# Kernel optimization log

Hardware: AMD Instinct MI355X
Metric: run time of the kernel (lower is better)

The kernel has to match this reference:

```python
import jax, jax.numpy as jnp
import numpy as np

NV, NE, D, NNZ = 100000, 50000, 128, 1600000
EPS = 1e-5

def _seg_mean(vals, idx, n):
    # vals: [nnz, d] gathered rows; mean-aggregate into n segments
    s = jax.ops.segment_sum(vals, idx, num_segments=n)
    c = jax.ops.segment_sum(jnp.ones((idx.shape[0], 1), vals.dtype), idx, num_segments=n)
    return s / jnp.maximum(c, 1.0)

def _linear(x, W, b):
    return x @ W.T + b

def _layer_norm(x, g, b):
    m = jnp.mean(x, axis=-1, keepdims=True)
    v = jnp.mean((x - m) ** 2, axis=-1, keepdims=True)
    return (x - m) * jax.lax.rsqrt(v + EPS) * g + b

def setup_inputs() -> dict:
    key = jax.random.key(0)
    ks = jax.random.split(key, 12)
    inp = {
        "X": jax.random.normal(ks[0], (NV, D), jnp.float32),
        "Y": jax.random.normal(ks[1], (NE, D), jnp.float32),
        "v_idx": jax.random.randint(ks[2], (NNZ,), 0, NV, jnp.int32),
        "e_idx": jax.random.randint(ks[3], (NNZ,), 0, NE, jnp.int32),
        "W_tv": jax.random.normal(ks[4], (D, D), jnp.float32) * 0.05,
        "b_tv": jnp.zeros((D,), jnp.float32),
        "W_te": jax.random.normal(ks[5], (D, D), jnp.float32) * 0.05,
        "b_te": jnp.zeros((D,), jnp.float32),
        "W_em": jax.random.normal(ks[6], (D, 2 * D), jnp.float32) * 0.05,
        "b_em": jnp.zeros((D,), jnp.float32),
        "W_vm": jax.random.normal(ks[7], (D, 2 * D), jnp.float32) * 0.05,
        "b_vm": jnp.zeros((D,), jnp.float32),
        "g_v": jnp.ones((D,), jnp.float32),
        "be_v": jnp.zeros((D,), jnp.float32),
        "g_e": jnp.ones((D,), jnp.float32),
        "be_e": jnp.zeros((D,), jnp.float32),
    }
    return inp

def reference(X, Y, v_idx, e_idx, W_tv, b_tv, W_te, b_te, W_em, b_em, W_vm, b_vm, g_v, be_v, g_e, be_e):
    X0, Y0 = X, Y
    Xp = _linear(X0, W_tv, b_tv)                       # [NV, D] theta_vertex
    # v2e aggregation (mean): gather vertex rows per incidence, reduce to edges
    msg_e = _seg_mean(Xp[v_idx], e_idx, NE)            # [NE, D]
    Ym = _linear(jnp.concatenate([Y0, msg_e], axis=-1), W_em, b_em)  # edge_merge
    Ym = _linear(Ym, W_te, b_te)                       # theta_edge
    # e2v aggregation (mean)
    msg_v = _seg_mean(Ym[e_idx], v_idx, NV)            # [NV, D]
    Xm = _linear(jnp.concatenate([X0, msg_v], axis=-1), W_vm, b_vm)  # vertex_merge
    Xo = jax.nn.relu(_layer_norm(Xm, g_v, be_v))       # dropout is identity at eval / p=0
    Yo = jax.nn.relu(_layer_norm(Ym, g_e, be_e))
    return (Xo, Yo)
```

## Files before the change

kernel.cpp:

```cpp
#include <hip/hip_runtime.h>
#include <stdint.h>

#define NVERT 100000
#define NEDGE 50000
#define DIM 128
#define NNZ_N 1600000
#define N4 (NNZ_N / 4)
#define CAP_E 96
#define CAP_V 56
#define NB_QTR 1563
#define NB_G23 782
#define MSG_STRIDE 256

typedef __attribute__((ext_vector_type(8))) short bf16x8;
typedef __attribute__((ext_vector_type(4))) float f32x4;

__device__ __forceinline__ unsigned short f32_to_bf16(float f) {
  union { float f; unsigned u; } v; v.f = f;
  unsigned r = v.u + 0x7fffu + ((v.u >> 16) & 1u);
  return (unsigned short)(r >> 16);
}
__device__ __forceinline__ float bf16_lo(unsigned u) {
  union { unsigned u; float f; } v; v.u = u << 16; return v.f;
}
__device__ __forceinline__ float bf16_hi(unsigned u) {
  union { unsigned u; float f; } v; v.u = u & 0xffff0000u; return v.f;
}
__device__ __forceinline__ float ldf(const void* p, long i, int bf) {
  if (bf) {
    union { unsigned u; float f; } v;
    v.u = (unsigned)((const unsigned short*)p)[i] << 16;
    return v.f;
  }
  return ((const float*)p)[i];
}
__device__ __forceinline__ bf16x8 frag_ext(const void* A, long idx, int bf) {
  if (bf) return *(const bf16x8*)((const unsigned short*)A + idx);
  const float* f = (const float*)A + idx;
  float4 f0 = *(const float4*)f, f1 = *(const float4*)(f + 4);
  bf16x8 r;
  r[0] = (short)f32_to_bf16(f0.x); r[1] = (short)f32_to_bf16(f0.y);
  r[2] = (short)f32_to_bf16(f0.z); r[3] = (short)f32_to_bf16(f0.w);
  r[4] = (short)f32_to_bf16(f1.x); r[5] = (short)f32_to_bf16(f1.y);
  r[6] = (short)f32_to_bf16(f1.z); r[7] = (short)f32_to_bf16(f1.w);
  return r;
}

__device__ __forceinline__ int block_flag(const unsigned short* x) {
  __shared__ int cnt;
  if (threadIdx.x == 0) cnt = 0;
  __syncthreads();
  int c = 0;
#pragma unroll
  for (int k = 0; k < 4; ++k) {
    unsigned short h = x[(threadIdx.x * 4 + k) * 2];
    int ex = (h >> 7) & 0xFF;
    c += (ex >= 100 && ex <= 140) ? 1 : 0;
  }
  atomicAdd(&cnt, c);
  __syncthreads();
  return cnt > 512;
}

__global__ __launch_bounds__(256) void prep0(
    const unsigned short* __restrict__ Xu,
    const void* __restrict__ btv, const void* __restrict__ bvm,
    const void* __restrict__ Wtv,
    float* __restrict__ btvf, float* __restrict__ bvmf,
    unsigned short* __restrict__ Wtvb, int* __restrict__ flag,
    int* __restrict__ cnt_e, int* __restrict__ cnt_v) {
  int b = blockIdx.x, t = threadIdx.x;
  if (b >= 65) {
    int i = (b - 65) * 256 + t;
    if (i < NEDGE) cnt_e[i] = 0;
    else if (i < NEDGE + NVERT) cnt_v[i - NEDGE] = 0;
    return;
  }
  int bf = block_flag(Xu);
  if (b == 0) {
    if (t == 0) flag[0] = bf;
    if (t < 128) btvf[t] = ldf(btv, t, bf);
    else bvmf[t - 128] = ldf(bvm, t - 128, bf);
  } else {
    int i = (b - 1) * 256 + t;
    Wtvb[i] = f32_to_bf16(ldf(Wtv, i, bf));
  }
}

__device__ __forceinline__ void prep_wc_body(
    int b, const void* __restrict__ Wvm, const void* __restrict__ Wte,
    const void* __restrict__ Wem, const void* __restrict__ bte,
    const void* __restrict__ bem, unsigned short* __restrict__ Wvmb,
    unsigned short* __restrict__ Wcb, float* __restrict__ bcf, int bf) {
  int t = threadIdx.x;
  if (b < 128) {
    int i = b * 256 + t;
    Wvmb[i] = f32_to_bf16(ldf(Wvm, i, bf));
  } else {
    int n = b - 128, k = t;
    float acc = 0.f;
    for (int j = 0; j < 128; ++j)
      acc += ldf(Wte, n * 128 + j, bf) * ldf(Wem, j * 256 + k, bf);
    Wcb[n * 256 + k] = f32_to_bf16(acc);
    if (k == 0) {
      float bb = ldf(bte, n, bf);
      for (int j = 0; j < 128; ++j) bb += ldf(Wte, n * 128 + j, bf) * ldf(bem, j, bf);
      bcf[n] = bb;
    }
  }
}

__device__ __forceinline__ void ecount_body(
    const int4* __restrict__ vi, const int4* __restrict__ ei,
    int* __restrict__ cnt_e, int* __restrict__ adj_e, int bid) {
  int i = bid * 256 + threadIdx.x;
  if (i >= N4) return;
  int4 e = ei[i], v = vi[i];
  int t;
  t = atomicAdd(&cnt_e[e.x], 1); if (t < CAP_E) adj_e[e.x * CAP_E + t] = v.x;
  t = atomicAdd(&cnt_e[e.y], 1); if (t < CAP_E) adj_e[e.y * CAP_E + t] = v.y;
  t = atomicAdd(&cnt_e[e.z], 1); if (t < CAP_E) adj_e[e.z * CAP_E + t] = v.z;
  t = atomicAdd(&cnt_e[e.w], 1); if (t < CAP_E) adj_e[e.w * CAP_E + t] = v.w;
}

__device__ __forceinline__ void vcount_body(
    const int4* __restrict__ vi, const int4* __restrict__ ei,
    int* __restrict__ cnt_v, unsigned short* __restrict__ adj_v, int bid) {
  int i = bid * 256 + threadIdx.x;
  if (i >= N4) return;
  int4 v = vi[i], e = ei[i];
  int t;
  t = atomicAdd(&cnt_v[v.x], 1); if (t < CAP_V) adj_v[v.x * CAP_V + t] = (unsigned short)e.x;
  t = atomicAdd(&cnt_v[v.y], 1); if (t < CAP_V) adj_v[v.y * CAP_V + t] = (unsigned short)e.y;
  t = atomicAdd(&cnt_v[v.z], 1); if (t < CAP_V) adj_v[v.z * CAP_V + t] = (unsigned short)e.z;
  t = atomicAdd(&cnt_v[v.w], 1); if (t < CAP_V) adj_v[v.w * CAP_V + t] = (unsigned short)e.w;
}

template<typename IT, int CAP>
__device__ __forceinline__ void seg_body(
    const int* __restrict__ cntp, const IT* __restrict__ adj,
    const unsigned short* __restrict__ tbl, unsigned short* __restrict__ out,
    int nseg, int nrows, int bid) {
  const int seg = (bid * 256 + threadIdx.x) >> 4;
  const int l = threadIdx.x & 15;
  if (seg >= nseg) return;
  int cnt = cntp[seg];
  int s = seg * CAP;
  int e = s + (cnt < CAP ? cnt : CAP);
  float a0 = 0, a1 = 0, a2 = 0, a3 = 0, a4 = 0, a5 = 0, a6 = 0, a7 = 0;
#define ROW(r, u)                                      \
  if ((unsigned)r >= (unsigned)nrows) r = 0;           \
  uint4 u = *(const uint4*)(tbl + (long)r * DIM + l * 8);
#define ACC(u)                                         \
  a0 += bf16_lo(u.x); a1 += bf16_hi(u.x);              \
  a2 += bf16_lo(u.y); a3 += bf16_hi(u.y);              \
  a4 += bf16_lo(u.z); a5 += bf16_hi(u.z);              \
  a6 += bf16_lo(u.w); a7 += bf16_hi(u.w);
  int i = s;
  for (; i + 8 <= e; i += 8) {
    int r0 = adj[i],     r1 = adj[i + 1], r2 = adj[i + 2], r3 = adj[i + 3];
    int r4 = adj[i + 4], r5 = adj[i + 5], r6 = adj[i + 6], r7 = adj[i + 7];
    ROW(r0, u0) ROW(r1, u1) ROW(r2, u2) ROW(r3, u3)
    ROW(r4, u4) ROW(r5, u5) ROW(r6, u6) ROW(r7, u7)
    ACC(u0) ACC(u1) ACC(u2) ACC(u3) ACC(u4) ACC(u5) ACC(u6) ACC(u7)
  }
  for (; i + 4 <= e; i += 4) {
    int r0 = adj[i], r1 = adj[i + 1], r2 = adj[i + 2], r3 = adj[i + 3];
    ROW(r0, u0) ROW(r1, u1) ROW(r2, u2) ROW(r3, u3)
    ACC(u0) ACC(u1) ACC(u2) ACC(u3)
  }
  for (; i < e; ++i) {
    int r = adj[i];
    ROW(r, u)
    ACC(u)
  }
#undef ACC
#undef ROW
  float inv = (cnt > 0) ? 1.f / (float)cnt : 0.f;
  bf16x8 r;
  r[0] = (short)f32_to_bf16(a0 * inv); r[1] = (short)f32_to_bf16(a1 * inv);
  r[2] = (short)f32_to_bf16(a2 * inv); r[3] = (short)f32_to_bf16(a3 * inv);
  r[4] = (short)f32_to_bf16(a4 * inv); r[5] = (short)f32_to_bf16(a5 * inv);
  r[6] = (short)f32_to_bf16(a6 * inv); r[7] = (short)f32_to_bf16(a7 * inv);
  *(bf16x8*)(out + (long)seg * MSG_STRIDE + l * 8) = r;
}

__device__ __forceinline__ void gemm1_body(
    int bid, const void* __restrict__ A0,
    const unsigned short* __restrict__ Bw, const float* __restrict__ biasf,
    unsigned short* __restrict__ outb, int M, int bf) {
  const int wave = threadIdx.x >> 6;
  const int lane = threadIdx.x & 63;
  const int m0 = bid * 64 + wave * 16;
  if (m0 >= M) return;
  const int c = lane & 15;
  const int q = lane >> 4;
  const long arow = m0 + c;
  f32x4 acc[8];
#pragma unroll
  for (int t = 0; t < 8; ++t) acc[t] = (f32x4){0.f, 0.f, 0.f, 0.f};
#pragma unroll
  for (int ks = 0; ks < 4; ++ks) {
    const int kk = ks * 32 + q * 8;
    bf16x8 a = frag_ext(A0, arow * 128 + kk, bf);
#pragma unroll
    for (int t = 0; t < 8; ++t) {
      bf16x8 b = *(const bf16x8*)(Bw + (long)(t * 16 + c) * 128 + kk);
      acc[t] = __builtin_amdgcn_mfma_f32_16x16x32_bf16(a, b, acc[t], 0, 0, 0);
    }
  }
#pragma unroll
  for (int t = 0; t < 8; ++t) {
    float bv = biasf[t * 16 + c];
    int col = t * 16 + c;
#pragma unroll
    for (int i = 0; i < 4; ++i)
      outb[(long)(m0 + q * 4 + i) * DIM + col] = f32_to_bf16(acc[t][i] + bv);
  }
}

template<bool STORE_BF16>
__device__ __forceinline__ void gemm23_body(
    int bid, int rowbase, int M,
    const void* __restrict__ A0, const unsigned short* __restrict__ A1b,
    const unsigned short* __restrict__ Bw, const float* __restrict__ biasf,
    unsigned short* __restrict__ outb, float* __restrict__ outf,
    const void* __restrict__ gw_, const void* __restrict__ bw_, int bf) {
  const int wave = threadIdx.x >> 6;
  const int lane = threadIdx.x & 63;
  const int m0 = rowbase + bid * 64 + wave * 16;
  if (m0 >= M) return;
  const int c = lane & 15;
  const int q = lane >> 4;
  const long arow = m0 + c;

  f32x4 acc[8];
#pragma unroll
  for (int t = 0; t < 8; ++t) acc[t] = (f32x4){0.f, 0.f, 0.f, 0.f};
#pragma unroll
  for (int ks = 0; ks < 8; ++ks) {
    const int kk = ks * 32 + q * 8;
    bf16x8 a;
    if (ks >= 4) a = *(const bf16x8*)(A1b + arow * MSG_STRIDE + (kk - 128));
    else         a = frag_ext(A0, arow * 128 + kk, bf);
#pragma unroll
    for (int t = 0; t < 8; ++t) {
      bf16x8 b = *(const bf16x8*)(Bw + (long)(t * 16 + c) * 256 + kk);
      acc[t] = __builtin_amdgcn_mfma_f32_16x16x32_bf16(a, b, acc[t], 0, 0, 0);
    }
  }
#pragma unroll
  for (int t = 0; t < 8; ++t) {
    float bv = biasf[t * 16 + c];
#pragma unroll
    for (int i = 0; i < 4; ++i) acc[t][i] += bv;
  }
  if (STORE_BF16) {
#pragma unroll
    for (int t = 0; t < 8; ++t) {
      int col = t * 16 + c;
#pragma unroll
      for (int i = 0; i < 4; ++i)
        outb[(long)(m0 + q * 4 + i) * DIM + col] = f32_to_bf16(acc[t][i]);
    }
  }
  float sum[4] = {0, 0, 0, 0}, sq[4] = {0, 0, 0, 0};
#pragma unroll
  for (int t = 0; t < 8; ++t)
#pragma unroll
    for (int i = 0; i < 4; ++i) { float v = acc[t][i]; sum[i] += v; sq[i] += v * v; }
#pragma unroll
  for (int m = 1; m <= 8; m <<= 1) {
#pragma unroll
    for (int i = 0; i < 4; ++i) {
      sum[i] += __shfl_xor(sum[i], m, 64);
      sq[i]  += __shfl_xor(sq[i], m, 64);
    }
  }
  float mean[4], rstd[4];
#pragma unroll
  for (int i = 0; i < 4; ++i) {
    mean[i] = sum[i] * (1.0f / 128.0f);
    float var = sq[i] * (1.0f / 128.0f) - mean[i] * mean[i];
    rstd[i] = rsqrtf(var + 1e-5f);
  }
#pragma unroll
  for (int t = 0; t < 8; ++t) {
    int col = t * 16 + c;
    float gv = ldf(gw_, col, bf), bv = ldf(bw_, col, bf);
#pragma unroll
    for (int i = 0; i < 4; ++i) {
      float v = (acc[t][i] - mean[i]) * rstd[i] * gv + bv;
      v = v > 0.f ? v : 0.f;
      outf[(long)(m0 + q * 4 + i) * DIM + col] = v;
    }
  }
}

__global__ __launch_bounds__(256) void k1_prep_ecount_gemm1(
    const int4* __restrict__ vi, const int4* __restrict__ ei,
    int* __restrict__ cnt_e, int* __restrict__ adj_e,
    const void* __restrict__ X, const unsigned short* __restrict__ Wtvb,
    const float* __restrict__ btvf, unsigned short* __restrict__ Xp_b,
    const void* __restrict__ Wvm, const void* __restrict__ Wte,
    const void* __restrict__ Wem, const void* __restrict__ bte,
    const void* __restrict__ bem, unsigned short* __restrict__ Wvmb,
    unsigned short* __restrict__ Wcb, float* __restrict__ bcf,
    const int* __restrict__ flagp) {
  int b = blockIdx.x;
  if (b < 256) {
    prep_wc_body(b, Wvm, Wte, Wem, bte, bem, Wvmb, Wcb, bcf, *flagp);
    return;
  }
  int b2 = b - 256;
  if (b2 & 1)
    gemm1_body(b2 >> 1, X, Wtvb, btvf, Xp_b, NVERT, *flagp);
  else
    ecount_body(vi, ei, cnt_e, adj_e, b2 >> 1);
}

__global__ __launch_bounds__(256) void k2_vcount_seg1(
    const int4* __restrict__ vi, const int4* __restrict__ ei,
    int* __restrict__ cnt_v, unsigned short* __restrict__ adj_v,
    const int* __restrict__ cnt_e, const int* __restrict__ adj_e,
    const unsigned short* __restrict__ Xp_b, unsigned short* __restrict__ msg_e) {
  int r = blockIdx.x % 3, q = blockIdx.x / 3;
  if (r == 0)
    vcount_body(vi, ei, cnt_v, adj_v, q);
  else
    seg_body<int, CAP_E>(cnt_e, adj_e, Xp_b, msg_e, NEDGE, NVERT,
                         q * 2 + (r - 1));
}

__global__ __launch_bounds__(256) void k3_gemm2(
    const void* __restrict__ Y, const unsigned short* __restrict__ msg_e,
    const unsigned short* __restrict__ Wcb, const float* __restrict__ bcf,
    unsigned short* __restrict__ Ym_b, float* __restrict__ Yo,
    const void* __restrict__ g_e, const void* __restrict__ be_e,
    const int* __restrict__ flagp) {
  gemm23_body<true>(blockIdx.x, 0, NEDGE, Y, msg_e, Wcb, bcf, Ym_b, Yo,
                    g_e, be_e, *flagp);
}

__global__ __launch_bounds__(256) void k4a_seg2(
    const int* __restrict__ cnt_v, const unsigned short* __restrict__ adj_v,
    const unsigned short* __restrict__ Ym_b, unsigned short* __restrict__ msg_v) {
  seg_body<unsigned short, CAP_V>(cnt_v, adj_v, Ym_b, msg_v, NVERT, NEDGE,
                                  blockIdx.x);
}

__global__ __launch_bounds__(256) void k4b_seg2_gemm3(
    const int* __restrict__ cnt_v, const unsigned short* __restrict__ adj_v,
    const unsigned short* __restrict__ Ym_b, unsigned short* __restrict__ msg_v,
    const void* __restrict__ X, const unsigned short* __restrict__ Wvmb,
    const float* __restrict__ bvmf, float* __restrict__ Xo,
    const void* __restrict__ g_v, const void* __restrict__ be_v,
    const int* __restrict__ flagp) {
  int r = blockIdx.x % 5, q = blockIdx.x / 5;
  if (r == 4)
    gemm23_body<false>(q, 0, NVERT / 2, X, msg_v, Wvmb, bvmf, nullptr, Xo,
                       g_v, be_v, *flagp);
  else
    seg_body<unsigned short, CAP_V>(cnt_v, adj_v, Ym_b, msg_v, NVERT, NEDGE,
                                    3125 + q * 4 + r);
}

__global__ __launch_bounds__(256) void k5_gemm3(
    const void* __restrict__ X, const unsigned short* __restrict__ msg_v,
    const unsigned short* __restrict__ Wvmb, const float* __restrict__ bvmf,
    float* __restrict__ Xo, const void* __restrict__ g_v,
    const void* __restrict__ be_v, const int* __restrict__ flagp) {
  gemm23_body<false>(blockIdx.x, NVERT / 2, NVERT, X, msg_v, Wvmb, bvmf,
                     nullptr, Xo, g_v, be_v, *flagp);
}

extern "C" void kernel_launch(void* const* d_in, const int* in_sizes, int n_in,
                              void* d_out, int out_size, void* d_ws, size_t ws_size,
                              hipStream_t stream) {
  const void* X    = d_in[0];
  const void* Y    = d_in[1];
  const int*  v_idx = (const int*)d_in[2];
  const int*  e_idx = (const int*)d_in[3];
  const void* W_tv = d_in[4];
  const void* b_tv = d_in[5];
  const void* W_te = d_in[6];
  const void* b_te = d_in[7];
  const void* W_em = d_in[8];
  const void* b_em = d_in[9];
  const void* W_vm = d_in[10];
  const void* b_vm = d_in[11];
  const void* g_v  = d_in[12];
  const void* be_v = d_in[13];
  const void* g_e  = d_in[14];
  const void* be_e = d_in[15];

  unsigned short* Xp_b  = (unsigned short*)d_out;
  int*   adj_e = (int*)((char*)d_out + 25600000);
  unsigned short* msg_e = (unsigned short*)((char*)d_out + 51200000);
  float* Yo    = (float*)((char*)d_out + 51200000);
  unsigned short* msg_v = (unsigned short*)d_out;
  float* Xo    = (float*)d_out;

  char* p = (char*)d_ws;
  auto alloc = [&](size_t n) { char* r = p; p += (n + 255) & ~(size_t)255; return r; };
  int*   flag  = (int*)alloc(4);
  float* btv_f = (float*)alloc(DIM * 4);
  float* bvm_f = (float*)alloc(DIM * 4);
  float* bc_f  = (float*)alloc(DIM * 4);
  unsigned short* Wtv_b = (unsigned short*)alloc(DIM * DIM * 2);
  unsigned short* Wvm_b = (unsigned short*)alloc(2 * DIM * DIM * 2);
  unsigned short* Wc_b  = (unsigned short*)alloc(2 * DIM * DIM * 2);
  unsigned short* Ym_b  = (unsigned short*)alloc((long)NEDGE * DIM * 2);
  int* cnt_e  = (int*)alloc(NEDGE * 4);
  int* cnt_v  = (int*)alloc(NVERT * 4);
  unsigned short* adj_v = (unsigned short*)alloc((long)NVERT * CAP_V * 2);

  prep0<<<65 + (NEDGE + NVERT + 255) / 256, 256, 0, stream>>>(
      (const unsigned short*)X, b_tv, b_vm, W_tv, btv_f, bvm_f, Wtv_b, flag,
      cnt_e, cnt_v);

  k1_prep_ecount_gemm1<<<256 + 2 * NB_QTR, 256, 0, stream>>>(
      (const int4*)v_idx, (const int4*)e_idx, cnt_e, adj_e,
      X, Wtv_b, btv_f, Xp_b,
      W_vm, W_te, W_em, b_te, b_em, Wvm_b, Wc_b, bc_f, flag);

  k2_vcount_seg1<<<3 * NB_QTR, 256, 0, stream>>>(
      (const int4*)v_idx, (const int4*)e_idx, cnt_v, adj_v,
      cnt_e, adj_e, Xp_b, msg_e);

  k3_gemm2<<<NB_G23, 256, 0, stream>>>(
      Y, msg_e, Wc_b, bc_f, Ym_b, Yo, g_e, be_e, flag);

  k4a_seg2<<<3125, 256, 0, stream>>>(cnt_v, adj_v, Ym_b, msg_v);

  k4b_seg2_gemm3<<<5 * NB_G23, 256, 0, stream>>>(
      cnt_v, adj_v, Ym_b, msg_v, X, Wvm_b, bvm_f, Xo, g_v, be_v, flag);

  k5_gemm3<<<NB_G23, 256, 0, stream>>>(
      X, msg_v, Wvm_b, bvm_f, Xo, g_v, be_v, flag);
}
```

Before: 523.1 us.

## Split vertex aggregation/merge into three staggered stages and vectorize adjacency loads

Splits the vertex-side segment aggregation and vertex-merge GEMM into three thirds. Each fused launch aggregates the next third of vertices while the GEMM processes the previous third, which shortens the serialized tail and adds one kernel launch. Adjacency indices in the gather loop are now read with 128-bit vector loads instead of scalar loads, and the 4-wide remainder loop is dropped. The atomics in the incidence-counting kernels are also issued back to back before the dependent stores, to overlap atomic latency.

```diff
diff --git a/kernel.cpp b/kernel.cpp
--- a/kernel.cpp
+++ b/kernel.cpp
@@ -11,6 +11,10 @@
 #define NB_QTR 1563
 #define NB_G23 782
 #define MSG_STRIDE 256
+#define SEG_T1 33344
+#define SEG_T2 66688
+#define SB3 2084
+#define GB3 521
 
 typedef __attribute__((ext_vector_type(8))) short bf16x8;
 typedef __attribute__((ext_vector_type(4))) float f32x4;
@@ -116,11 +120,14 @@
   int i = bid * 256 + threadIdx.x;
   if (i >= N4) return;
   int4 e = ei[i], v = vi[i];
-  int t;
-  t = atomicAdd(&cnt_e[e.x], 1); if (t < CAP_E) adj_e[e.x * CAP_E + t] = v.x;
-  t = atomicAdd(&cnt_e[e.y], 1); if (t < CAP_E) adj_e[e.y * CAP_E + t] = v.y;
-  t = atomicAdd(&cnt_e[e.z], 1); if (t < CAP_E) adj_e[e.z * CAP_E + t] = v.z;
-  t = atomicAdd(&cnt_e[e.w], 1); if (t < CAP_E) adj_e[e.w * CAP_E + t] = v.w;
+  int t0 = atomicAdd(&cnt_e[e.x], 1);
+  int t1 = atomicAdd(&cnt_e[e.y], 1);
+  int t2 = atomicAdd(&cnt_e[e.z], 1);
+  int t3 = atomicAdd(&cnt_e[e.w], 1);
+  if (t0 < CAP_E) adj_e[e.x * CAP_E + t0] = v.x;
+  if (t1 < CAP_E) adj_e[e.y * CAP_E + t1] = v.y;
+  if (t2 < CAP_E) adj_e[e.z * CAP_E + t2] = v.z;
+  if (t3 < CAP_E) adj_e[e.w * CAP_E + t3] = v.w;
 }
 
 __device__ __forceinline__ void vcount_body(
@@ -129,11 +136,14 @@
   int i = bid * 256 + threadIdx.x;
   if (i >= N4) return;
   int4 v = vi[i], e = ei[i];
-  int t;
-  t = atomicAdd(&cnt_v[v.x], 1); if (t < CAP_V) adj_v[v.x * CAP_V + t] = (unsigned short)e.x;
-  t = atomicAdd(&cnt_v[v.y], 1); if (t < CAP_V) adj_v[v.y * CAP_V + t] = (unsigned short)e.y;
-  t = atomicAdd(&cnt_v[v.z], 1); if (t < CAP_V) adj_v[v.z * CAP_V + t] = (unsigned short)e.z;
-  t = atomicAdd(&cnt_v[v.w], 1); if (t < CAP_V) adj_v[v.w * CAP_V + t] = (unsigned short)e.w;
+  int t0 = atomicAdd(&cnt_v[v.x], 1);
+  int t1 = atomicAdd(&cnt_v[v.y], 1);
+  int t2 = atomicAdd(&cnt_v[v.z], 1);
+  int t3 = atomicAdd(&cnt_v[v.w], 1);
+  if (t0 < CAP_V) adj_v[v.x * CAP_V + t0] = (unsigned short)e.x;
+  if (t1 < CAP_V) adj_v[v.y * CAP_V + t1] = (unsigned short)e.y;
+  if (t2 < CAP_V) adj_v[v.z * CAP_V + t2] = (unsigned short)e.z;
+  if (t3 < CAP_V) adj_v[v.w * CAP_V + t3] = (unsigned short)e.w;
 }
 
 template<typename IT, int CAP>
@@ -158,19 +168,25 @@
   a6 += bf16_lo(u.w); a7 += bf16_hi(u.w);
   int i = s;
   for (; i + 8 <= e; i += 8) {
-    int r0 = adj[i],     r1 = adj[i + 1], r2 = adj[i + 2], r3 = adj[i + 3];
-    int r4 = adj[i + 4], r5 = adj[i + 5], r6 = adj[i + 6], r7 = adj[i + 7];
+    int r0, r1, r2, r3, r4, r5, r6, r7;
+    if constexpr (sizeof(IT) == 2) {
+      uint4 A = *(const uint4*)((const unsigned short*)adj + i);
+      r0 = (int)(A.x & 0xffffu); r1 = (int)(A.x >> 16);
+      r2 = (int)(A.y & 0xffffu); r3 = (int)(A.y >> 16);
+      r4 = (int)(A.z & 0xffffu); r5 = (int)(A.z >> 16);
+      r6 = (int)(A.w & 0xffffu); r7 = (int)(A.w >> 16);
+    } else {
+      int4 A = *(const int4*)((const int*)adj + i);
+      int4 B = *(const int4*)((const int*)adj + i + 4);
+      r0 = A.x; r1 = A.y; r2 = A.z; r3 = A.w;
+      r4 = B.x; r5 = B.y; r6 = B.z; r7 = B.w;
+    }
     ROW(r0, u0) ROW(r1, u1) ROW(r2, u2) ROW(r3, u3)
     ROW(r4, u4) ROW(r5, u5) ROW(r6, u6) ROW(r7, u7)
     ACC(u0) ACC(u1) ACC(u2) ACC(u3) ACC(u4) ACC(u5) ACC(u6) ACC(u7)
   }
-  for (; i + 4 <= e; i += 4) {
-    int r0 = adj[i], r1 = adj[i + 1], r2 = adj[i + 2], r3 = adj[i + 3];
-    ROW(r0, u0) ROW(r1, u1) ROW(r2, u2) ROW(r3, u3)
-    ACC(u0) ACC(u1) ACC(u2) ACC(u3)
-  }
   for (; i < e; ++i) {
-    int r = adj[i];
+    int r = (int)adj[i];
     ROW(r, u)
     ACC(u)
   }
@@ -345,11 +361,12 @@
 __global__ __launch_bounds__(256) void k4a_seg2(
     const int* __restrict__ cnt_v, const unsigned short* __restrict__ adj_v,
     const unsigned short* __restrict__ Ym_b, unsigned short* __restrict__ msg_v) {
-  seg_body<unsigned short, CAP_V>(cnt_v, adj_v, Ym_b, msg_v, NVERT, NEDGE,
+  seg_body<unsigned short, CAP_V>(cnt_v, adj_v, Ym_b, msg_v, SEG_T1, NEDGE,
                                   blockIdx.x);
 }
 
-__global__ __launch_bounds__(256) void k4b_seg2_gemm3(
+__global__ __launch_bounds__(256) void k4_seg2_gemm3(
+    int segblk_base, int nseg, int rowbase, int M,
     const int* __restrict__ cnt_v, const unsigned short* __restrict__ adj_v,
     const unsigned short* __restrict__ Ym_b, unsigned short* __restrict__ msg_v,
     const void* __restrict__ X, const unsigned short* __restrict__ Wvmb,
@@ -358,11 +375,11 @@
     const int* __restrict__ flagp) {
   int r = blockIdx.x % 5, q = blockIdx.x / 5;
   if (r == 4)
-    gemm23_body<false>(q, 0, NVERT / 2, X, msg_v, Wvmb, bvmf, nullptr, Xo,
+    gemm23_body<false>(q, rowbase, M, X, msg_v, Wvmb, bvmf, nullptr, Xo,
                        g_v, be_v, *flagp);
   else
-    seg_body<unsigned short, CAP_V>(cnt_v, adj_v, Ym_b, msg_v, NVERT, NEDGE,
-                                    3125 + q * 4 + r);
+    seg_body<unsigned short, CAP_V>(cnt_v, adj_v, Ym_b, msg_v, nseg, NEDGE,
+                                    segblk_base + q * 4 + r);
 }
 
 __global__ __launch_bounds__(256) void k5_gemm3(
@@ -370,7 +387,7 @@
     const unsigned short* __restrict__ Wvmb, const float* __restrict__ bvmf,
     float* __restrict__ Xo, const void* __restrict__ g_v,
     const void* __restrict__ be_v, const int* __restrict__ flagp) {
-  gemm23_body<false>(blockIdx.x, NVERT / 2, NVERT, X, msg_v, Wvmb, bvmf,
+  gemm23_body<false>(blockIdx.x, SEG_T2, NVERT, X, msg_v, Wvmb, bvmf,
                      nullptr, Xo, g_v, be_v, *flagp);
 }
 
@@ -431,11 +448,16 @@
   k3_gemm2<<<NB_G23, 256, 0, stream>>>(
       Y, msg_e, Wc_b, bc_f, Ym_b, Yo, g_e, be_e, flag);
 
-  k4a_seg2<<<3125, 256, 0, stream>>>(cnt_v, adj_v, Ym_b, msg_v);
-
-  k4b_seg2_gemm3<<<5 * NB_G23, 256, 0, stream>>>(
+  k4a_seg2<<<SB3, 256, 0, stream>>>(cnt_v, adj_v, Ym_b, msg_v);
+
+  k4_seg2_gemm3<<<5 * GB3, 256, 0, stream>>>(
+      SB3, SEG_T2, 0, SEG_T1,
       cnt_v, adj_v, Ym_b, msg_v, X, Wvm_b, bvm_f, Xo, g_v, be_v, flag);
 
-  k5_gemm3<<<NB_G23, 256, 0, stream>>>(
+  k4_seg2_gemm3<<<5 * GB3, 256, 0, stream>>>(
+      2 * SB3, NVERT, SEG_T1, SEG_T2,
+      cnt_v, adj_v, Ym_b, msg_v, X, Wvm_b, bvm_f, Xo, g_v, be_v, flag);
+
+  k5_gemm3<<<GB3, 256, 0, stream>>>(
       X, msg_v, Wvm_b, bvm_f, Xo, g_v, be_v, flag);
 }
```

Result: slower. 552.8 us (+5.7%).
